# Kernel tuning notes

Measured on AMD Instinct MI355X. Metric: run time of the kernel, lower is better.

## Reference

```python
import jax, jax.numpy as jnp
import numpy as np

C_M, C_Z, N_HEADS = 256, 128, 8
HEAD_DIM = C_M // N_HEADS
EPS = 1e-5


def _layer_norm(x, scale, bias):
    mu = jnp.mean(x, axis=-1, keepdims=True)
    var = jnp.mean(jnp.square(x - mu), axis=-1, keepdims=True)
    return (x - mu) * jax.lax.rsqrt(var + EPS) * scale + bias


def setup_inputs() -> dict:
    key = jax.random.key(0)
    ks = jax.random.split(key, 12)
    N, L = 128, 256
    s_m = 1.0 / np.sqrt(C_M)
    s_z = 1.0 / np.sqrt(C_Z)
    return {
        "msa": jax.random.normal(ks[0], (N, L, C_M), dtype=jnp.float32),
        "pair": jax.random.normal(ks[1], (L, L, C_Z), dtype=jnp.float32),
        "ln_m_scale": jnp.ones((C_M,), jnp.float32),
        "ln_m_bias": jnp.zeros((C_M,), jnp.float32),
        "ln_z_scale": jnp.ones((C_Z,), jnp.float32),
        "ln_z_bias": jnp.zeros((C_Z,), jnp.float32),
        "w_q": jax.random.normal(ks[2], (C_M, C_M), jnp.float32) * s_m,
        "w_k": jax.random.normal(ks[3], (C_M, C_M), jnp.float32) * s_m,
        "w_v": jax.random.normal(ks[4], (C_M, C_M), jnp.float32) * s_m,
        "w_b": jax.random.normal(ks[5], (N_HEADS, C_Z), jnp.float32) * s_z,
        "w_out": jax.random.normal(ks[6], (C_M, C_M), jnp.float32) * s_m,
        "b_out": jnp.zeros((C_M,), jnp.float32),
        "w_gate": jax.random.normal(ks[7], (C_M, C_M), jnp.float32) * s_m,
        "b_gate": jnp.zeros((C_M,), jnp.float32),
    }


def reference(msa, pair, ln_m_scale, ln_m_bias, ln_z_scale, ln_z_bias,
              w_q, w_k, w_v, w_b, w_out, b_out, w_gate, b_gate):
    N, L, _ = msa.shape
    m = _layer_norm(msa, ln_m_scale, ln_m_bias)          # (N, L, c_m)
    z = _layer_norm(pair, ln_z_scale, ln_z_bias)         # (L, L, c_z)
    q = (m @ w_q.T).reshape(N, L, N_HEADS, HEAD_DIM)
    k = (m @ w_k.T).reshape(N, L, N_HEADS, HEAD_DIM)
    v = (m @ w_v.T).reshape(N, L, N_HEADS, HEAD_DIM)
    attn = jnp.einsum('bihd,bjhd->bhij', q, k) / np.sqrt(HEAD_DIM).astype(np.float32)
    bias = jnp.einsum('ijc,hc->hij', z, w_b)             # (H, L, L)
    attn = jax.nn.softmax(attn + bias[None], axis=-1)    # (N, H, L, L)
    out = jnp.einsum('bhij,bjhd->bihd', attn, v).reshape(N, L, C_M)
    return msa + jax.nn.sigmoid(m @ w_gate.T + b_gate) * (out @ w_out.T + b_out)
```

## Files before the change

kernel.cpp:

```cpp
#include <hip/hip_runtime.h>

typedef unsigned short u16;
typedef float f32x4 __attribute__((ext_vector_type(4)));
typedef __bf16 bf16x8 __attribute__((ext_vector_type(8)));

__device__ __forceinline__ u16 f2bf(float f) {
  union { float f; unsigned u; } v; v.f = f;
  unsigned r = (v.u + 0x7fffu + ((v.u >> 16) & 1u)) >> 16;
  return (u16)r;
}
__device__ __forceinline__ float bf2f(u16 h) {
  union { unsigned u; float f; } v; v.u = ((unsigned)h) << 16; return v.f;
}

#define GLOAD16(gp, lp)                                                        \
  __builtin_amdgcn_global_load_lds(                                            \
      (const __attribute__((address_space(1))) void*)(gp),                     \
      (__attribute__((address_space(3))) void*)(lp), 16, 0, 0)

#define LOG2E 1.4426950408889634f
#define HS 1048576

__global__ __launch_bounds__(256) void pre_kernel(
    const float* __restrict__ x, const float* __restrict__ sc,
    const float* __restrict__ bi, u16* __restrict__ mo,
    const float* __restrict__ wq, const float* __restrict__ wk,
    const float* __restrict__ wv, const float* __restrict__ wg,
    const float* __restrict__ wo, u16* __restrict__ wcat, u16* __restrict__ wobf,
    const float* __restrict__ pair, const float* __restrict__ scz,
    const float* __restrict__ biz, const float* __restrict__ wb,
    u16* __restrict__ biasQ)
{
  __shared__ float swc[1024];
  __shared__ float sA[8], sB2[8];
  const int tid = threadIdx.x;

  if (blockIdx.x < 8192) {
    const int row  = blockIdx.x * 4 + (tid >> 6);
    const int lane = tid & 63;
    const float4 v = *(const float4*)(x + (size_t)row * 256 + lane * 4);
    float s = v.x + v.y + v.z + v.w;
    #pragma unroll
    for (int off = 1; off < 64; off <<= 1) s += __shfl_xor(s, off);
    const float mu = s * 0.00390625f;
    const float d0 = v.x - mu, d1 = v.y - mu, d2 = v.z - mu, d3 = v.w - mu;
    float vs = d0*d0 + d1*d1 + d2*d2 + d3*d3;
    #pragma unroll
    for (int off = 1; off < 64; off <<= 1) vs += __shfl_xor(vs, off);
    const float rstd = rsqrtf(vs * 0.00390625f + 1e-5f);
    const float4 scv = *(const float4*)(sc + lane * 4);
    const float4 biv = *(const float4*)(bi + lane * 4);
    ushort4 o;
    o.x = f2bf(d0 * rstd * scv.x + biv.x);
    o.y = f2bf(d1 * rstd * scv.y + biv.y);
    o.z = f2bf(d2 * rstd * scv.z + biv.z);
    o.w = f2bf(d3 * rstd * scv.w + biv.w);
    *(ushort4*)(mo + (size_t)row * 256 + lane * 4) = o;
  } else if (blockIdx.x < 8512) {
    int idx = (blockIdx.x - 8192) * 256 + tid;
    int e = idx * 4;
    int row = e >> 8;
    int col = e & 255;
    const float* src = (row < 256)  ? (wq + (size_t)row * 256)
                     : (row < 512)  ? (wk + (size_t)(row - 256) * 256)
                     : (row < 768)  ? (wv + (size_t)(row - 512) * 256)
                     : (row < 1024) ? (wg + (size_t)(row - 768) * 256)
                                    : (wo + (size_t)(row - 1024) * 256);
    float4 v = *(const float4*)(src + col);
    ushort4 o;
    o.x = f2bf(v.x); o.y = f2bf(v.y); o.z = f2bf(v.z); o.w = f2bf(v.w);
    if (row < 1024) *(ushort4*)(wcat + e) = o;
    else            *(ushort4*)(wobf + (e - 262144)) = o;
  } else {
    #pragma unroll
    for (int k = 0; k < 4; ++k) {
      int idx = k * 256 + tid;
      int c = idx >> 3, h = idx & 7;
      swc[idx] = scz[c] * wb[h * 128 + c];
    }
    __syncthreads();
    if (tid < 8) {
      float a = 0.f, b2 = 0.f;
      for (int c = 0; c < 128; ++c) {
        a  += swc[c * 8 + tid];
        b2 += biz[c] * wb[tid * 128 + c];
      }
      sA[tid] = a; sB2[tid] = b2;
    }
    __syncthreads();
    const int gt = (blockIdx.x - 8512) * 256 + tid;
    const int ij = gt >> 1, hg = gt & 1;
    const float* xr = pair + (size_t)ij * 128;
    float s = 0.f, ss = 0.f;
    float d0 = 0.f, d1 = 0.f, d2 = 0.f, d3 = 0.f;
    for (int c0 = 0; c0 < 128; c0 += 4) {
      float4 xv4 = *(const float4*)(xr + c0);
      float xe[4] = {xv4.x, xv4.y, xv4.z, xv4.w};
      #pragma unroll
      for (int e = 0; e < 4; ++e) {
        const float xv = xe[e];
        s += xv; ss += xv * xv;
        const f32x4 wv = *(const f32x4*)&swc[(c0 + e) * 8 + hg * 4];
        d0 += xv * wv[0]; d1 += xv * wv[1];
        d2 += xv * wv[2]; d3 += xv * wv[3];
      }
    }
    const float mu = s * 0.0078125f;
    const float rstd = rsqrtf(ss * 0.0078125f - mu * mu + 1e-5f);
    const int i = ij >> 8, j = ij & 255;
    const float dd[4] = {d0, d1, d2, d3};
    #pragma unroll
    for (int hh = 0; hh < 4; ++hh) {
      const int h = hg * 4 + hh;
      const float bias = (dd[hh] - mu * sA[h]) * rstd + sB2[h];
      biasQ[h * 65536 + i * 256 + j] = f2bf(bias * LOG2E);
    }
  }
}

template<int EPI, int NCG>
__global__ __launch_bounds__(256, 4) void gemm_bstat(
    const u16* __restrict__ A, const u16* __restrict__ B,
    u16* __restrict__ qh, u16* __restrict__ kh, u16* __restrict__ vh,
    u16* __restrict__ gateb, const float* __restrict__ bgate,
    float* __restrict__ Cf, const float* __restrict__ msa,
    const float* __restrict__ bout)
{
  __shared__ u16 sB[64 * 256];
  const int tid = threadIdx.x, lane = tid & 63, w = tid >> 6;
  const int g = lane >> 4, r15 = lane & 15;
  const int x = blockIdx.x & 7;
  const int j = blockIdx.x >> 3;
  const int cg = j % NCG;
  const int rpl = j / NCG;
  const int bcol = cg * 64;

  #pragma unroll
  for (int i = 0; i < 8; ++i) {
    int c = i * 256 + tid;
    int col = c >> 5, s = c & 31;
    int lc = (s & 24) | ((s ^ col) & 7);
    GLOAD16(B + (size_t)(bcol + col) * 256 + lc * 8, &sB[c * 8]);
  }

  float gb[4] = {0.f, 0.f, 0.f, 0.f};
  if (EPI == 0 && cg >= (NCG * 3) / 4) {
    #pragma unroll
    for (int n = 0; n < 4; ++n) gb[n] = bgate[bcol - 768 + n * 16 + r15];
  }
  float bo[4] = {0.f, 0.f, 0.f, 0.f};
  if (EPI == 1) {
    #pragma unroll
    for (int n = 0; n < 4; ++n) bo[n] = bout[bcol + n * 16 + r15];
  }

  const size_t brow = ((size_t)(x * 32) + rpl) * 128;
  bf16x8 af[2][8];
  #pragma unroll
  for (int m = 0; m < 2; ++m) {
    const size_t arow = brow + w * 32 + m * 16 + r15;
    #pragma unroll
    for (int kk = 0; kk < 8; ++kk)
      af[m][kk] = *(const bf16x8*)(A + arow * 256 + kk * 32 + g * 8);
  }
  __syncthreads();

  f32x4 acc[2][4] = {};
  #pragma unroll
  for (int kk = 0; kk < 8; ++kk) {
    bf16x8 bfr[4];
    #pragma unroll
    for (int n = 0; n < 4; ++n) {
      int col = n * 16 + r15;
      int lcq = kk * 4 + g;
      int s = (lcq & 24) | ((lcq ^ col) & 7);
      bfr[n] = *(const bf16x8*)&sB[col * 256 + s * 8];
    }
    #pragma unroll
    for (int m = 0; m < 2; ++m)
      #pragma unroll
      for (int n = 0; n < 4; ++n)
        acc[m][n] = __builtin_amdgcn_mfma_f32_16x16x32_bf16(af[m][kk], bfr[n], acc[m][n], 0, 0, 0);
  }

  if (EPI == 0) {
    __syncthreads();
    #pragma unroll
    for (int m = 0; m < 2; ++m) {
      const int lr0 = w * 32 + m * 16 + g * 4;
      #pragma unroll
      for (int n = 0; n < 4; ++n) {
        const int colL = n * 16 + r15;
        #pragma unroll
        for (int rr = 0; rr < 4; ++rr) {
          float v = acc[m][n][rr];
          if (cg < NCG / 4) v *= 0.17677669529663687f * LOG2E;
          else if (cg >= (NCG * 3) / 4)
            v = 1.0f / (1.0f + __expf(-(v + gb[n])));
          sB[(lr0 + rr) * 72 + colL] = f2bf(v);
        }
      }
    }
    __syncthreads();
    #pragma unroll
    for (int i = 0; i < 4; ++i) {
      const int c = i * 256 + tid;
      const int lr = c >> 3, cc = (c & 7) * 8;
      const size_t rowg = brow + lr;
      const uint4 vv = *(const uint4*)&sB[lr * 72 + cc];
      const int colg = bcol + cc;
      if (cg < NCG / 4) {
        *(uint4*)(qh + (size_t)(colg >> 5) * HS + rowg * 32 + (colg & 31)) = vv;
      } else if (cg < NCG / 2) {
        const int c2 = colg - 256;
        *(uint4*)(kh + (size_t)(c2 >> 5) * HS + rowg * 32 + (c2 & 31)) = vv;
      } else if (cg < (NCG * 3) / 4) {
        const int c2 = colg - 512;
        *(uint4*)(vh + (size_t)(c2 >> 5) * HS + rowg * 32 + (c2 & 31)) = vv;
      } else {
        *(uint4*)(gateb + rowg * 256 + (colg - 768)) = vv;
      }
    }
  } else {
    #pragma unroll
    for (int m = 0; m < 2; ++m) {
      const int row0 = (int)brow + w * 32 + m * 16 + g * 4;
      #pragma unroll
      for (int n = 0; n < 4; ++n) {
        const int col = bcol + n * 16 + r15;
        #pragma unroll
        for (int rr = 0; rr < 4; ++rr) {
          float v = acc[m][n][rr] + bo[n];
          const size_t orow = (size_t)(row0 + rr);
          float gg = bf2f(gateb[orow * 256 + col]);
          Cf[orow * 256 + col] = msa[orow * 256 + col] + gg * v;
        }
      }
    }
  }
}

__global__ __launch_bounds__(256) void attn_kernel(
    const u16* __restrict__ qh, const u16* __restrict__ kh,
    const u16* __restrict__ vh, const u16* __restrict__ biasQ,
    u16* __restrict__ attn_out)
{
  __shared__ u16 sVt[32 * 264];
  const int blk = blockIdx.x;
  const int h = blk & 7;
  const int idx2 = blk >> 3;
  const int qh_i = idx2 & 1;
  const int b = idx2 >> 1;
  const int tid = threadIdx.x, lane = tid & 63, w = tid >> 6;
  const int g = lane >> 4, r15 = lane & 15;
  const size_t rowbase = (size_t)b * 256;
  const int qbase = qh_i * 128;

  const u16* Qh = qh + (size_t)h * HS;
  const u16* Kh = kh + (size_t)h * HS;
  const u16* Vh = vh + (size_t)h * HS;

  {
    const int nl = (tid >> 4) & 3, q4 = tid & 15;
    const int pos = (tid >> 6) * 64 + (nl >> 1) * 32 + (q4 >> 2) * 8 + (nl & 1) * 4 + (q4 & 3);
    const uint4* vr4 = (const uint4*)(Vh + (rowbase + tid) * 32);
    #pragma unroll
    for (int c = 0; c < 4; ++c) {
      uint4 vv = vr4[c];
      unsigned uu[4] = {vv.x, vv.y, vv.z, vv.w};
      #pragma unroll
      for (int p = 0; p < 4; ++p) {
        sVt[(c * 8 + p * 2    ) * 264 + pos] = (u16)(uu[p] & 0xffffu);
        sVt[(c * 8 + p * 2 + 1) * 264 + pos] = (u16)(uu[p] >> 16);
      }
    }
  }

  const int qrel0 = qbase + w * 32 + r15;
  bf16x8 qf[2];
  #pragma unroll
  for (int m = 0; m < 2; ++m)
    qf[m] = *(const bf16x8*)(Qh + (rowbase + qrel0 + m * 16) * 32 + g * 8);
  __syncthreads();

  f32x4 oacc[2][2] = {};
  float lrun[2] = {0.f, 0.f};
  const u16* biasH = biasQ + (size_t)h * 65536;

  bf16x8 kf[4];
  ushort4 bvu[2][4];
  #pragma unroll
  for (int n = 0; n < 4; ++n)
    kf[n] = *(const bf16x8*)(Kh + (rowbase + n * 16 + r15) * 32 + g * 8);
  #pragma unroll
  for (int m = 0; m < 2; ++m)
    #pragma unroll
    for (int n = 0; n < 4; ++n)
      bvu[m][n] = *(const ushort4*)(biasH + (size_t)(qrel0 + m * 16) * 256 + n * 16 + g * 4);

  for (int jb = 0; jb < 4; ++jb) {
    f32x4 s[2][4];
    #pragma unroll
    for (int m = 0; m < 2; ++m) {
      #pragma unroll
      for (int n = 0; n < 4; ++n) {
        f32x4 z = {0.f, 0.f, 0.f, 0.f};
        s[m][n] = __builtin_amdgcn_mfma_f32_16x16x32_bf16(kf[n], qf[m], z, 0, 0, 0);
        const u16* bb = (const u16*)&bvu[m][n];
        #pragma unroll
        for (int rr = 0; rr < 4; ++rr) s[m][n][rr] += bf2f(bb[rr]);
      }
    }
    if (jb < 3) {
      const int j1 = jb + 1;
      #pragma unroll
      for (int n = 0; n < 4; ++n)
        kf[n] = *(const bf16x8*)(Kh + (rowbase + j1 * 64 + n * 16 + r15) * 32 + g * 8);
      #pragma unroll
      for (int m = 0; m < 2; ++m)
        #pragma unroll
        for (int n = 0; n < 4; ++n)
          bvu[m][n] = *(const ushort4*)(biasH + (size_t)(qrel0 + m * 16) * 256 + j1 * 64 + n * 16 + g * 4);
    }
    #pragma unroll
    for (int m = 0; m < 2; ++m)
      #pragma unroll
      for (int n = 0; n < 4; ++n)
        #pragma unroll
        for (int rr = 0; rr < 4; ++rr) {
          float p = __builtin_amdgcn_exp2f(s[m][n][rr]);
          s[m][n][rr] = p;
          lrun[m] += p;
        }
    #pragma unroll
    for (int kb = 0; kb < 2; ++kb) {
      bf16x8 vt[2];
      #pragma unroll
      for (int nd = 0; nd < 2; ++nd)
        vt[nd] = *(const bf16x8*)&sVt[(nd * 16 + r15) * 264 + jb * 64 + kb * 32 + g * 8];
      #pragma unroll
      for (int m = 0; m < 2; ++m) {
        bf16x8 pv;
        #pragma unroll
        for (int rr = 0; rr < 4; ++rr) {
          pv[rr]     = (__bf16)s[m][2 * kb][rr];
          pv[4 + rr] = (__bf16)s[m][2 * kb + 1][rr];
        }
        #pragma unroll
        for (int nd = 0; nd < 2; ++nd)
          oacc[m][nd] = __builtin_amdgcn_mfma_f32_16x16x32_bf16(pv, vt[nd], oacc[m][nd], 0, 0, 0);
      }
    }
  }

  #pragma unroll
  for (int m = 0; m < 2; ++m) {
    float l = lrun[m];
    l += __shfl_xor(l, 16);
    l += __shfl_xor(l, 32);
    const float inv = 1.0f / l;
    #pragma unroll
    for (int rr = 0; rr < 4; ++rr) {
      const float invq = __shfl(inv, g * 4 + rr);
      const size_t qrow = rowbase + qbase + w * 32 + m * 16 + g * 4 + rr;
      #pragma unroll
      for (int nd = 0; nd < 2; ++nd)
        attn_out[qrow * 256 + h * 32 + nd * 16 + r15] = f2bf(oacc[m][nd][rr] * invq);
    }
  }
}

extern "C" void kernel_launch(void* const* d_in, const int* in_sizes, int n_in,
                              void* d_out, int out_size, void* d_ws, size_t ws_size,
                              hipStream_t stream)
{
  (void)in_sizes; (void)n_in; (void)out_size; (void)ws_size;
  const float* msa        = (const float*)d_in[0];
  const float* pair       = (const float*)d_in[1];
  const float* ln_m_scale = (const float*)d_in[2];
  const float* ln_m_bias  = (const float*)d_in[3];
  const float* ln_z_scale = (const float*)d_in[4];
  const float* ln_z_bias  = (const float*)d_in[5];
  const float* w_q        = (const float*)d_in[6];
  const float* w_k        = (const float*)d_in[7];
  const float* w_v        = (const float*)d_in[8];
  const float* w_b        = (const float*)d_in[9];
  const float* w_out      = (const float*)d_in[10];
  const float* b_out      = (const float*)d_in[11];
  const float* w_gate     = (const float*)d_in[12];
  const float* b_gate     = (const float*)d_in[13];

  char* ws = (char*)d_ws;
  u16*   m_bf   = (u16*)(ws);
  u16*   wcat   = (u16*)(ws + 16777216);
  u16*   wobf   = (u16*)(ws + 17301504);
  u16*   qh     = (u16*)(ws + 17432576);
  u16*   kh     = (u16*)(ws + 34209792);
  u16*   vh     = (u16*)(ws + 50987008);
  u16*   gateb  = (u16*)(ws + 67764224);
  u16*   biasQ  = (u16*)(ws + 84541440);
  u16*   attn_o = (u16*)(ws + 86638592);
  float* out = (float*)d_out;

  pre_kernel<<<dim3(9024), dim3(256), 0, stream>>>(
      msa, ln_m_scale, ln_m_bias, m_bf, w_q, w_k, w_v, w_gate, w_out, wcat, wobf,
      pair, ln_z_scale, ln_z_bias, w_b, biasQ);
  gemm_bstat<0, 16><<<dim3(4096), dim3(256), 0, stream>>>(m_bf, wcat, qh, kh, vh, gateb,
                                                          b_gate, nullptr, nullptr, nullptr);
  attn_kernel<<<dim3(2048), dim3(256), 0, stream>>>(qh, kh, vh, biasQ, attn_o);
  gemm_bstat<1, 4><<<dim3(1024), dim3(256), 0, stream>>>(attn_o, wobf, nullptr, nullptr, nullptr,
                                                         gateb, nullptr, out, msa, b_out);
}
```

Before: 141.1 us.

## Fuse QKV/gate projection into attention kernel with per-head weight fragments

Merges the QKV+gate projection GEMM with the attention kernel. Each 512-thread block handles one (sequence, head) pair: it computes that head's Q, K, V and gate slices directly into LDS from pre-swizzled MFMA weight fragments, then runs attention from LDS. This removes the global round trip of the q/k/v intermediates and one kernel launch. In exchange, each block recomputes nothing but reloads the full 256-row A tile for every head (8x A reads). The block also uses more LDS and launches fewer, larger blocks, which may lower occupancy. Gate and attention outputs now use a head-major layout, and the output GEMM is changed to read that layout.

```diff
diff --git a/kernel.cpp b/kernel.cpp
--- a/kernel.cpp
+++ b/kernel.cpp
@@ -26,7 +26,7 @@
     const float* __restrict__ bi, u16* __restrict__ mo,
     const float* __restrict__ wq, const float* __restrict__ wk,
     const float* __restrict__ wv, const float* __restrict__ wg,
-    const float* __restrict__ wo, u16* __restrict__ wcat, u16* __restrict__ wobf,
+    const float* __restrict__ wo, u16* __restrict__ wfrag, u16* __restrict__ wobf,
     const float* __restrict__ pair, const float* __restrict__ scz,
     const float* __restrict__ biz, const float* __restrict__ wb,
     u16* __restrict__ biasQ)
@@ -56,21 +56,28 @@
     o.z = f2bf(d2 * rstd * scv.z + biv.z);
     o.w = f2bf(d3 * rstd * scv.w + biv.w);
     *(ushort4*)(mo + (size_t)row * 256 + lane * 4) = o;
-  } else if (blockIdx.x < 8512) {
-    int idx = (blockIdx.x - 8192) * 256 + tid;
-    int e = idx * 4;
-    int row = e >> 8;
-    int col = e & 255;
-    const float* src = (row < 256)  ? (wq + (size_t)row * 256)
-                     : (row < 512)  ? (wk + (size_t)(row - 256) * 256)
-                     : (row < 768)  ? (wv + (size_t)(row - 512) * 256)
-                     : (row < 1024) ? (wg + (size_t)(row - 768) * 256)
-                                    : (wo + (size_t)(row - 1024) * 256);
-    float4 v = *(const float4*)(src + col);
+  } else if (blockIdx.x < 9216) {
+    const int d4 = (blockIdx.x - 8192) * 256 + tid;
+    const int e0 = (d4 & 1) * 4;
+    const int lane = (d4 >> 1) & 63;
+    const int n  = (d4 >> 7) & 1;
+    const int W  = (d4 >> 8) & 3;
+    const int kk = (d4 >> 10) & 7;
+    const int h  = (d4 >> 13) & 7;
+    const float* src = (W == 0) ? wq : (W == 1) ? wk : (W == 2) ? wv : wg;
+    const int row = h * 32 + n * 16 + (lane & 15);
+    const int col = kk * 32 + (lane >> 4) * 8 + e0;
+    float4 v = *(const float4*)(src + (size_t)row * 256 + col);
     ushort4 o;
     o.x = f2bf(v.x); o.y = f2bf(v.y); o.z = f2bf(v.z); o.w = f2bf(v.w);
-    if (row < 1024) *(ushort4*)(wcat + e) = o;
-    else            *(ushort4*)(wobf + (e - 262144)) = o;
+    *(ushort4*)(wfrag + ((((((size_t)h * 8 + kk) * 4 + W) * 2 + n) * 64 + lane) * 8 + e0)) = o;
+  } else if (blockIdx.x < 9280) {
+    int e = ((blockIdx.x - 9216) * 256 + tid) * 4;
+    int row = e >> 8, col = e & 255;
+    float4 v = *(const float4*)(wo + (size_t)row * 256 + col);
+    ushort4 o;
+    o.x = f2bf(v.x); o.y = f2bf(v.y); o.z = f2bf(v.z); o.w = f2bf(v.w);
+    *(ushort4*)(wobf + e) = o;
   } else {
     #pragma unroll
     for (int k = 0; k < 4; ++k) {
@@ -88,7 +95,7 @@
       sA[tid] = a; sB2[tid] = b2;
     }
     __syncthreads();
-    const int gt = (blockIdx.x - 8512) * 256 + tid;
+    const int gt = (blockIdx.x - 9280) * 256 + tid;
     const int ij = gt >> 1, hg = gt & 1;
     const float* xr = pair + (size_t)ij * 128;
     float s = 0.f, ss = 0.f;
@@ -118,180 +125,125 @@
   }
 }
 
-template<int EPI, int NCG>
-__global__ __launch_bounds__(256, 4) void gemm_bstat(
-    const u16* __restrict__ A, const u16* __restrict__ B,
-    u16* __restrict__ qh, u16* __restrict__ kh, u16* __restrict__ vh,
-    u16* __restrict__ gateb, const float* __restrict__ bgate,
-    float* __restrict__ Cf, const float* __restrict__ msa,
-    const float* __restrict__ bout)
+__global__ __launch_bounds__(512) void qkv_attn_kernel(
+    const u16* __restrict__ A, const u16* __restrict__ wfrag,
+    const float* __restrict__ bgate, const u16* __restrict__ biasQ,
+    u16* __restrict__ gatebh, u16* __restrict__ attn_oh)
 {
-  __shared__ u16 sB[64 * 256];
+  __shared__ u16 Qlds[256 * 40];
+  __shared__ u16 Klds[256 * 40];
+  __shared__ u16 sVt[32 * 264];
   const int tid = threadIdx.x, lane = tid & 63, w = tid >> 6;
   const int g = lane >> 4, r15 = lane & 15;
-  const int x = blockIdx.x & 7;
-  const int j = blockIdx.x >> 3;
-  const int cg = j % NCG;
-  const int rpl = j / NCG;
-  const int bcol = cg * 64;
-
-  #pragma unroll
-  for (int i = 0; i < 8; ++i) {
-    int c = i * 256 + tid;
-    int col = c >> 5, s = c & 31;
-    int lc = (s & 24) | ((s ^ col) & 7);
-    GLOAD16(B + (size_t)(bcol + col) * 256 + lc * 8, &sB[c * 8]);
-  }
-
-  float gb[4] = {0.f, 0.f, 0.f, 0.f};
-  if (EPI == 0 && cg >= (NCG * 3) / 4) {
-    #pragma unroll
-    for (int n = 0; n < 4; ++n) gb[n] = bgate[bcol - 768 + n * 16 + r15];
-  }
-  float bo[4] = {0.f, 0.f, 0.f, 0.f};
-  if (EPI == 1) {
-    #pragma unroll
-    for (int n = 0; n < 4; ++n) bo[n] = bout[bcol + n * 16 + r15];
-  }
-
-  const size_t brow = ((size_t)(x * 32) + rpl) * 128;
+  const int h = blockIdx.x & 7;
+  const int b = blockIdx.x >> 3;
+  const size_t rowbase = (size_t)b * 256;
+
   bf16x8 af[2][8];
   #pragma unroll
   for (int m = 0; m < 2; ++m) {
-    const size_t arow = brow + w * 32 + m * 16 + r15;
+    const size_t arow = rowbase + w * 32 + m * 16 + r15;
     #pragma unroll
     for (int kk = 0; kk < 8; ++kk)
       af[m][kk] = *(const bf16x8*)(A + arow * 256 + kk * 32 + g * 8);
   }
+
+  const u16* wfh = wfrag + (size_t)h * 32768;
+
+  #define PROJ(Wi, ACC)                                                        \
+    {                                                                          \
+      _Pragma("unroll")                                                        \
+      for (int m = 0; m < 2; ++m)                                              \
+        _Pragma("unroll")                                                      \
+        for (int n = 0; n < 2; ++n) ACC[m][n] = (f32x4){0.f, 0.f, 0.f, 0.f};   \
+      _Pragma("unroll")                                                        \
+      for (int kk = 0; kk < 8; ++kk) {                                         \
+        bf16x8 wf0 = *(const bf16x8*)(wfh + ((kk * 4 + Wi) * 2 + 0) * 512 + lane * 8); \
+        bf16x8 wf1 = *(const bf16x8*)(wfh + ((kk * 4 + Wi) * 2 + 1) * 512 + lane * 8); \
+        _Pragma("unroll")                                                      \
+        for (int m = 0; m < 2; ++m) {                                          \
+          ACC[m][0] = __builtin_amdgcn_mfma_f32_16x16x32_bf16(wf0, af[m][kk], ACC[m][0], 0, 0, 0); \
+          ACC[m][1] = __builtin_amdgcn_mfma_f32_16x16x32_bf16(wf1, af[m][kk], ACC[m][1], 0, 0, 0); \
+        }                                                                      \
+      }                                                                        \
+    }
+
+  f32x4 acc[2][2];
+
+  PROJ(3, acc);
+  {
+    const f32x4 gb0 = *(const f32x4*)(bgate + h * 32 + g * 4);
+    const f32x4 gb1 = *(const f32x4*)(bgate + h * 32 + 16 + g * 4);
+    #pragma unroll
+    for (int m = 0; m < 2; ++m)
+      #pragma unroll
+      for (int n = 0; n < 2; ++n) {
+        const f32x4 gb = (n == 0) ? gb0 : gb1;
+        ushort4 o;
+        o.x = f2bf(1.0f / (1.0f + __expf(-(acc[m][n][0] + gb[0]))));
+        o.y = f2bf(1.0f / (1.0f + __expf(-(acc[m][n][1] + gb[1]))));
+        o.z = f2bf(1.0f / (1.0f + __expf(-(acc[m][n][2] + gb[2]))));
+        o.w = f2bf(1.0f / (1.0f + __expf(-(acc[m][n][3] + gb[3]))));
+        *(ushort4*)&Qlds[(w * 32 + m * 16 + r15) * 40 + n * 16 + g * 4] = o;
+      }
+  }
   __syncthreads();
-
-  f32x4 acc[2][4] = {};
-  #pragma unroll
-  for (int kk = 0; kk < 8; ++kk) {
-    bf16x8 bfr[4];
-    #pragma unroll
-    for (int n = 0; n < 4; ++n) {
-      int col = n * 16 + r15;
-      int lcq = kk * 4 + g;
-      int s = (lcq & 24) | ((lcq ^ col) & 7);
-      bfr[n] = *(const bf16x8*)&sB[col * 256 + s * 8];
-    }
-    #pragma unroll
-    for (int m = 0; m < 2; ++m)
-      #pragma unroll
-      for (int n = 0; n < 4; ++n)
-        acc[m][n] = __builtin_amdgcn_mfma_f32_16x16x32_bf16(af[m][kk], bfr[n], acc[m][n], 0, 0, 0);
-  }
-
-  if (EPI == 0) {
-    __syncthreads();
-    #pragma unroll
-    for (int m = 0; m < 2; ++m) {
-      const int lr0 = w * 32 + m * 16 + g * 4;
-      #pragma unroll
-      for (int n = 0; n < 4; ++n) {
-        const int colL = n * 16 + r15;
-        #pragma unroll
-        for (int rr = 0; rr < 4; ++rr) {
-          float v = acc[m][n][rr];
-          if (cg < NCG / 4) v *= 0.17677669529663687f * LOG2E;
-          else if (cg >= (NCG * 3) / 4)
-            v = 1.0f / (1.0f + __expf(-(v + gb[n])));
-          sB[(lr0 + rr) * 72 + colL] = f2bf(v);
-        }
-      }
-    }
-    __syncthreads();
-    #pragma unroll
-    for (int i = 0; i < 4; ++i) {
-      const int c = i * 256 + tid;
-      const int lr = c >> 3, cc = (c & 7) * 8;
-      const size_t rowg = brow + lr;
-      const uint4 vv = *(const uint4*)&sB[lr * 72 + cc];
-      const int colg = bcol + cc;
-      if (cg < NCG / 4) {
-        *(uint4*)(qh + (size_t)(colg >> 5) * HS + rowg * 32 + (colg & 31)) = vv;
-      } else if (cg < NCG / 2) {
-        const int c2 = colg - 256;
-        *(uint4*)(kh + (size_t)(c2 >> 5) * HS + rowg * 32 + (c2 & 31)) = vv;
-      } else if (cg < (NCG * 3) / 4) {
-        const int c2 = colg - 512;
-        *(uint4*)(vh + (size_t)(c2 >> 5) * HS + rowg * 32 + (c2 & 31)) = vv;
-      } else {
-        *(uint4*)(gateb + rowg * 256 + (colg - 768)) = vv;
-      }
-    }
-  } else {
-    #pragma unroll
-    for (int m = 0; m < 2; ++m) {
-      const int row0 = (int)brow + w * 32 + m * 16 + g * 4;
-      #pragma unroll
-      for (int n = 0; n < 4; ++n) {
-        const int col = bcol + n * 16 + r15;
-        #pragma unroll
-        for (int rr = 0; rr < 4; ++rr) {
-          float v = acc[m][n][rr] + bo[n];
-          const size_t orow = (size_t)(row0 + rr);
-          float gg = bf2f(gateb[orow * 256 + col]);
-          Cf[orow * 256 + col] = msa[orow * 256 + col] + gg * v;
-        }
-      }
-    }
-  }
-}
-
-__global__ __launch_bounds__(256) void attn_kernel(
-    const u16* __restrict__ qh, const u16* __restrict__ kh,
-    const u16* __restrict__ vh, const u16* __restrict__ biasQ,
-    u16* __restrict__ attn_out)
-{
-  __shared__ u16 sVt[32 * 264];
-  const int blk = blockIdx.x;
-  const int h = blk & 7;
-  const int idx2 = blk >> 3;
-  const int qh_i = idx2 & 1;
-  const int b = idx2 >> 1;
-  const int tid = threadIdx.x, lane = tid & 63, w = tid >> 6;
-  const int g = lane >> 4, r15 = lane & 15;
-  const size_t rowbase = (size_t)b * 256;
-  const int qbase = qh_i * 128;
-
-  const u16* Qh = qh + (size_t)h * HS;
-  const u16* Kh = kh + (size_t)h * HS;
-  const u16* Vh = vh + (size_t)h * HS;
-
-  {
-    const int nl = (tid >> 4) & 3, q4 = tid & 15;
-    const int pos = (tid >> 6) * 64 + (nl >> 1) * 32 + (q4 >> 2) * 8 + (nl & 1) * 4 + (q4 & 3);
-    const uint4* vr4 = (const uint4*)(Vh + (rowbase + tid) * 32);
-    #pragma unroll
-    for (int c = 0; c < 4; ++c) {
-      uint4 vv = vr4[c];
-      unsigned uu[4] = {vv.x, vv.y, vv.z, vv.w};
-      #pragma unroll
-      for (int p = 0; p < 4; ++p) {
-        sVt[(c * 8 + p * 2    ) * 264 + pos] = (u16)(uu[p] & 0xffffu);
-        sVt[(c * 8 + p * 2 + 1) * 264 + pos] = (u16)(uu[p] >> 16);
-      }
-    }
-  }
-
-  const int qrel0 = qbase + w * 32 + r15;
+  #pragma unroll
+  for (int i = 0; i < 4; ++i) {
+    const int c = i * 512 + tid;
+    const int row = c >> 3, cc = (c & 7) * 4;
+    *(ushort4*)(gatebh + (size_t)h * HS + (rowbase + row) * 32 + cc) =
+        *(const ushort4*)&Qlds[row * 40 + cc];
+  }
+  __syncthreads();
+
+  PROJ(0, acc);
+  #pragma unroll
+  for (int m = 0; m < 2; ++m)
+    #pragma unroll
+    for (int n = 0; n < 2; ++n) {
+      ushort4 o;
+      o.x = f2bf(acc[m][n][0] * (0.17677669529663687f * LOG2E));
+      o.y = f2bf(acc[m][n][1] * (0.17677669529663687f * LOG2E));
+      o.z = f2bf(acc[m][n][2] * (0.17677669529663687f * LOG2E));
+      o.w = f2bf(acc[m][n][3] * (0.17677669529663687f * LOG2E));
+      *(ushort4*)&Qlds[(w * 32 + m * 16 + r15) * 40 + n * 16 + g * 4] = o;
+    }
+
+  PROJ(1, acc);
+  #pragma unroll
+  for (int m = 0; m < 2; ++m)
+    #pragma unroll
+    for (int n = 0; n < 2; ++n) {
+      ushort4 o;
+      o.x = f2bf(acc[m][n][0]); o.y = f2bf(acc[m][n][1]);
+      o.z = f2bf(acc[m][n][2]); o.w = f2bf(acc[m][n][3]);
+      *(ushort4*)&Klds[(w * 32 + m * 16 + r15) * 40 + n * 16 + g * 4] = o;
+    }
+
+  PROJ(2, acc);
+  #pragma unroll
+  for (int m = 0; m < 2; ++m) {
+    const int pos = (w >> 1) * 64 + (w & 1) * 32 + (r15 >> 2) * 8 + m * 4 + (r15 & 3);
+    #pragma unroll
+    for (int n = 0; n < 2; ++n)
+      #pragma unroll
+      for (int jj = 0; jj < 4; ++jj)
+        sVt[(n * 16 + g * 4 + jj) * 264 + pos] = f2bf(acc[m][n][jj]);
+  }
+  __syncthreads();
+
+  const int qrel0 = w * 32 + r15;
   bf16x8 qf[2];
   #pragma unroll
   for (int m = 0; m < 2; ++m)
-    qf[m] = *(const bf16x8*)(Qh + (rowbase + qrel0 + m * 16) * 32 + g * 8);
-  __syncthreads();
+    qf[m] = *(const bf16x8*)&Qlds[(qrel0 + m * 16) * 40 + g * 8];
 
   f32x4 oacc[2][2] = {};
   float lrun[2] = {0.f, 0.f};
   const u16* biasH = biasQ + (size_t)h * 65536;
 
-  bf16x8 kf[4];
   ushort4 bvu[2][4];
-  #pragma unroll
-  for (int n = 0; n < 4; ++n)
-    kf[n] = *(const bf16x8*)(Kh + (rowbase + n * 16 + r15) * 32 + g * 8);
   #pragma unroll
   for (int m = 0; m < 2; ++m)
     #pragma unroll
@@ -299,6 +251,10 @@
       bvu[m][n] = *(const ushort4*)(biasH + (size_t)(qrel0 + m * 16) * 256 + n * 16 + g * 4);
 
   for (int jb = 0; jb < 4; ++jb) {
+    bf16x8 kf[4];
+    #pragma unroll
+    for (int n = 0; n < 4; ++n)
+      kf[n] = *(const bf16x8*)&Klds[(jb * 64 + n * 16 + r15) * 40 + g * 8];
     f32x4 s[2][4];
     #pragma unroll
     for (int m = 0; m < 2; ++m) {
@@ -313,9 +269,6 @@
     }
     if (jb < 3) {
       const int j1 = jb + 1;
-      #pragma unroll
-      for (int n = 0; n < 4; ++n)
-        kf[n] = *(const bf16x8*)(Kh + (rowbase + j1 * 64 + n * 16 + r15) * 32 + g * 8);
       #pragma unroll
       for (int m = 0; m < 2; ++m)
         #pragma unroll
@@ -362,10 +315,82 @@
     #pragma unroll
     for (int rr = 0; rr < 4; ++rr) {
       const float invq = __shfl(inv, g * 4 + rr);
-      const size_t qrow = rowbase + qbase + w * 32 + m * 16 + g * 4 + rr;
+      const size_t qrow = rowbase + w * 32 + m * 16 + g * 4 + rr;
       #pragma unroll
       for (int nd = 0; nd < 2; ++nd)
-        attn_out[qrow * 256 + h * 32 + nd * 16 + r15] = f2bf(oacc[m][nd][rr] * invq);
+        attn_oh[(size_t)h * HS + qrow * 32 + nd * 16 + r15] = f2bf(oacc[m][nd][rr] * invq);
+    }
+  }
+}
+
+__global__ __launch_bounds__(256, 4) void gemm_epi1(
+    const u16* __restrict__ attn_oh, const u16* __restrict__ B,
+    const u16* __restrict__ gatebh, float* __restrict__ Cf,
+    const float* __restrict__ msa, const float* __restrict__ bout)
+{
+  __shared__ u16 sB[64 * 256];
+  const int tid = threadIdx.x, lane = tid & 63, w = tid >> 6;
+  const int g = lane >> 4, r15 = lane & 15;
+  const int x = blockIdx.x & 7;
+  const int j = blockIdx.x >> 3;
+  const int cg = j % 4;
+  const int rpl = j / 4;
+  const int bcol = cg * 64;
+
+  #pragma unroll
+  for (int i = 0; i < 8; ++i) {
+    int c = i * 256 + tid;
+    int col = c >> 5, s = c & 31;
+    int lc = (s & 24) | ((s ^ col) & 7);
+    GLOAD16(B + (size_t)(bcol + col) * 256 + lc * 8, &sB[c * 8]);
+  }
+
+  float bo[4];
+  #pragma unroll
+  for (int n = 0; n < 4; ++n) bo[n] = bout[bcol + n * 16 + r15];
+
+  const size_t brow = ((size_t)(x * 32) + rpl) * 128;
+  bf16x8 af[2][8];
+  #pragma unroll
+  for (int m = 0; m < 2; ++m) {
+    const size_t arow = brow + w * 32 + m * 16 + r15;
+    #pragma unroll
+    for (int kk = 0; kk < 8; ++kk)
+      af[m][kk] = *(const bf16x8*)(attn_oh + (size_t)kk * HS + arow * 32 + g * 8);
+  }
+  __syncthreads();
+
+  f32x4 acc[2][4] = {};
+  #pragma unroll
+  for (int kk = 0; kk < 8; ++kk) {
+    bf16x8 bfr[4];
+    #pragma unroll
+    for (int n = 0; n < 4; ++n) {
+      int col = n * 16 + r15;
+      int lcq = kk * 4 + g;
+      int s = (lcq & 24) | ((lcq ^ col) & 7);
+      bfr[n] = *(const bf16x8*)&sB[col * 256 + s * 8];
+    }
+    #pragma unroll
+    for (int m = 0; m < 2; ++m)
+      #pragma unroll
+      for (int n = 0; n < 4; ++n)
+        acc[m][n] = __builtin_amdgcn_mfma_f32_16x16x32_bf16(af[m][kk], bfr[n], acc[m][n], 0, 0, 0);
+  }
+
+  #pragma unroll
+  for (int m = 0; m < 2; ++m) {
+    const int row0 = (int)brow + w * 32 + m * 16 + g * 4;
+    #pragma unroll
+    for (int n = 0; n < 4; ++n) {
+      const int col = bcol + n * 16 + r15;
+      #pragma unroll
+      for (int rr = 0; rr < 4; ++rr) {
+        float v = acc[m][n][rr] + bo[n];
+        const size_t orow = (size_t)(row0 + rr);
+        float gg = bf2f(gatebh[(size_t)(col >> 5) * HS + orow * 32 + (col & 31)]);
+        Cf[orow * 256 + col] = msa[orow * 256 + col] + gg * v;
+      }
     }
   }
 }
@@ -391,23 +416,18 @@
   const float* b_gate     = (const float*)d_in[13];
 
   char* ws = (char*)d_ws;
-  u16*   m_bf   = (u16*)(ws);
-  u16*   wcat   = (u16*)(ws + 16777216);
-  u16*   wobf   = (u16*)(ws + 17301504);
-  u16*   qh     = (u16*)(ws + 17432576);
-  u16*   kh     = (u16*)(ws + 34209792);
-  u16*   vh     = (u16*)(ws + 50987008);
-  u16*   gateb  = (u16*)(ws + 67764224);
-  u16*   biasQ  = (u16*)(ws + 84541440);
-  u16*   attn_o = (u16*)(ws + 86638592);
+  u16*   m_bf    = (u16*)(ws);
+  u16*   wobf    = (u16*)(ws + 16777216);
+  u16*   wfrag   = (u16*)(ws + 16908288);
+  u16*   gatebh  = (u16*)(ws + 17432576);
+  u16*   biasQ   = (u16*)(ws + 34209792);
+  u16*   attn_oh = (u16*)(ws + 35258368);
   float* out = (float*)d_out;
 
-  pre_kernel<<<dim3(9024), dim3(256), 0, stream>>>(
-      msa, ln_m_scale, ln_m_bias, m_bf, w_q, w_k, w_v, w_gate, w_out, wcat, wobf,
+  pre_kernel<<<dim3(9792), dim3(256), 0, stream>>>(
+      msa, ln_m_scale, ln_m_bias, m_bf, w_q, w_k, w_v, w_gate, w_out, wfrag, wobf,
       pair, ln_z_scale, ln_z_bias, w_b, biasQ);
-  gemm_bstat<0, 16><<<dim3(4096), dim3(256), 0, stream>>>(m_bf, wcat, qh, kh, vh, gateb,
-                                                          b_gate, nullptr, nullptr, nullptr);
-  attn_kernel<<<dim3(2048), dim3(256), 0, stream>>>(qh, kh, vh, biasQ, attn_o);
-  gemm_bstat<1, 4><<<dim3(1024), dim3(256), 0, stream>>>(attn_o, wobf, nullptr, nullptr, nullptr,
-                                                         gateb, nullptr, out, msa, b_out);
-}
+  qkv_attn_kernel<<<dim3(1024), dim3(512), 0, stream>>>(
+      m_bf, wfrag, b_gate, biasQ, gatebh, attn_oh);
+  gemm_epi1<<<dim3(1024), dim3(256), 0, stream>>>(attn_oh, wobf, gatebh, out, msa, b_out);
+}
```

After: 143.1 us. Within noise of the previous version (+1.4%).
